# Kernel tuning notes

Hardware: AMD Instinct MI355X
Metric: run time of the kernel (lower is better)

Reference implementation:

```python
import jax, jax.numpy as jnp
import numpy as np


def setup_inputs() -> dict:
    key = jax.random.key(0)
    kq, kk, kv = jax.random.split(key, 3)
    n, m, d, v = 4096, 4096, 1024, 1024
    Q = jax.random.normal(kq, (n, d), dtype=jnp.float32)
    K = jax.random.normal(kk, (m, d), dtype=jnp.float32)
    V = jax.random.normal(kv, (m, v), dtype=jnp.float32)
    return {"Q": Q, "K": K, "V": V}


def reference(Q, K, V):
    d = K.shape[-1]
    scale = d ** (-0.5)
    logits = jnp.matmul(Q, K.T)                      # [n, m]
    # Faithful to source: softmax over dim=1 (keys), THEN scaled by d**-0.5
    scores = jax.nn.softmax(logits, axis=1) * scale  # [n, m]
    return jnp.matmul(scores, V)                     # [n, v]
```

## Files before the change

kernel.cpp:

```cpp
#include <hip/hip_runtime.h>
#include <hip/hip_bf16.h>

typedef _Float16 f16x8 __attribute__((ext_vector_type(8)));
typedef _Float16 f16x4 __attribute__((ext_vector_type(4)));
typedef float f32x4 __attribute__((ext_vector_type(4)));

__device__ __forceinline__ void async_ld16(_Float16* lds, const _Float16* g) {
    __builtin_amdgcn_global_load_lds(
        (const __attribute__((address_space(1))) void*)g,
        (__attribute__((address_space(3))) void*)lds, 16, 0, 0);
}

__global__ __launch_bounds__(256) void gemm_bt(
    const _Float16* __restrict__ A,
    const _Float16* __restrict__ B,
    float* __restrict__ C,
    int M, int N, int K, int Ks)
{
    __shared__ _Float16 At[2][128 * 32];
    __shared__ _Float16 Bt[2][128 * 32];

    const int tid  = threadIdx.x;
    const int wave = tid >> 6;
    const int lane = tid & 63;

    int gx = gridDim.x, gy = gridDim.y;
    int bx = blockIdx.x, by = blockIdx.y;
    if (((gx & 7) == 0) && ((gy & 7) == 0)) {
        const int bid    = bx + gx * by;
        const int ntx    = gx >> 3;
        const int sid    = bid >> 6;
        const int within = bid & 63;
        const int sx = sid % ntx;
        const int sy = sid / ntx;
        bx = (sx << 3) + (within & 7);
        by = (sy << 3) + (within >> 3);
    }
    const int row0 = by * 128;
    const int col0 = bx * 128;

    const int wr = (wave >> 1) * 64;
    const int wc = (wave & 1) * 64;
    const int quad = lane >> 4;
    const int l16  = lane & 15;

    f32x4 acc[4][4] = {};

    const int srow  = lane >> 2;
    const int skoff = (lane & 3) * 8;
    const size_t K64 = (size_t)64 * K;

    const _Float16* Ab = A + (size_t)row0 * K + (size_t)blockIdx.z * Ks;
    const _Float16* Bb = B + (size_t)col0 * K + (size_t)blockIdx.z * Ks;
    float* Cb = C + (size_t)blockIdx.z * M * N;

    const _Float16* pa = Ab + (size_t)(wave * 16 + srow) * K + skoff;
    const _Float16* pb = Bb + (size_t)(wave * 16 + srow) * K + skoff;

    async_ld16(At[0] + wave * 512,       pa);
    async_ld16(At[0] + (wave + 4) * 512, pa + K64);
    async_ld16(Bt[0] + wave * 512,       pb);
    async_ld16(Bt[0] + (wave + 4) * 512, pb + K64);
    __syncthreads();

    int cur = 0;
    for (int k0 = 0; k0 < Ks; k0 += 32) {
        const int nxt = cur ^ 1;
        if (k0 + 32 < Ks) {
            const _Float16* qa = pa + k0 + 32;
            const _Float16* qb = pb + k0 + 32;
            async_ld16(At[nxt] + wave * 512,       qa);
            async_ld16(At[nxt] + (wave + 4) * 512, qa + K64);
            async_ld16(Bt[nxt] + wave * 512,       qb);
            async_ld16(Bt[nxt] + (wave + 4) * 512, qb + K64);
        }

        f16x8 af[4], bf[4];
        #pragma unroll
        for (int r = 0; r < 4; ++r)
            af[r] = *(const f16x8*)&At[cur][(wr + r * 16 + l16) * 32 + quad * 8];
        #pragma unroll
        for (int c = 0; c < 4; ++c)
            bf[c] = *(const f16x8*)&Bt[cur][(wc + c * 16 + l16) * 32 + quad * 8];

        #pragma unroll
        for (int r = 0; r < 4; ++r)
            #pragma unroll
            for (int c = 0; c < 4; ++c)
                acc[r][c] = __builtin_amdgcn_mfma_f32_16x16x32_f16(af[r], bf[c], acc[r][c], 0, 0, 0);

        __syncthreads();
        cur = nxt;
    }

    #pragma unroll
    for (int r = 0; r < 4; ++r) {
        const int growb = row0 + wr + r * 16 + quad * 4;
        #pragma unroll
        for (int c = 0; c < 4; ++c) {
            const int gcol = col0 + wc + c * 16 + l16;
            #pragma unroll
            for (int i = 0; i < 4; ++i)
                Cb[(size_t)(growb + i) * N + gcol] = acc[r][c][i];
        }
    }
}

__global__ __launch_bounds__(256) void softmax_rows(
    const float* __restrict__ S, _Float16* __restrict__ P, float scale)
{
    __shared__ float red[4];
    const int row = blockIdx.x;
    const int tid = threadIdx.x;
    const int wave = tid >> 6;
    const float4* Sr = (const float4*)(S + (size_t)row * 4096);

    float4 x[4];
    #pragma unroll
    for (int i = 0; i < 4; ++i) x[i] = Sr[tid + i * 256];

    float mx = -3.402823466e+38f;
    #pragma unroll
    for (int i = 0; i < 4; ++i)
        mx = fmaxf(mx, fmaxf(fmaxf(x[i].x, x[i].y), fmaxf(x[i].z, x[i].w)));
    #pragma unroll
    for (int off = 32; off > 0; off >>= 1) mx = fmaxf(mx, __shfl_down(mx, off));
    if ((tid & 63) == 0) red[wave] = mx;
    __syncthreads();
    mx = fmaxf(fmaxf(red[0], red[1]), fmaxf(red[2], red[3]));
    __syncthreads();

    float sum = 0.0f;
    #pragma unroll
    for (int i = 0; i < 4; ++i) {
        x[i].x = __expf(x[i].x - mx);
        x[i].y = __expf(x[i].y - mx);
        x[i].z = __expf(x[i].z - mx);
        x[i].w = __expf(x[i].w - mx);
        sum += x[i].x + x[i].y + x[i].z + x[i].w;
    }
    #pragma unroll
    for (int off = 32; off > 0; off >>= 1) sum += __shfl_down(sum, off);
    if ((tid & 63) == 0) red[wave] = sum;
    __syncthreads();
    sum = red[0] + red[1] + red[2] + red[3];

    const float inv = scale / sum;
    f16x4* Pr = (f16x4*)(P + (size_t)row * 4096);
    #pragma unroll
    for (int i = 0; i < 4; ++i) {
        f16x4 h;
        h.x = (_Float16)(x[i].x * inv);
        h.y = (_Float16)(x[i].y * inv);
        h.z = (_Float16)(x[i].z * inv);
        h.w = (_Float16)(x[i].w * inv);
        Pr[tid + i * 256] = h;
    }
}

__global__ __launch_bounds__(256) void cvt2_f32_f16(
    const float4* __restrict__ a, f16x4* __restrict__ da, int n4a,
    const float4* __restrict__ b, f16x4* __restrict__ db, int n4b)
{
    int i = blockIdx.x * 256 + threadIdx.x;
    const int stride = gridDim.x * 256;
    const int tot = n4a + n4b;
    for (; i < tot; i += stride) {
        const float4* s = (i < n4a) ? (a + i) : (b + (i - n4a));
        f16x4* d = (i < n4a) ? (da + i) : (db + (i - n4a));
        float4 v = *s;
        f16x4 h;
        h.x = (_Float16)v.x; h.y = (_Float16)v.y;
        h.z = (_Float16)v.z; h.w = (_Float16)v.w;
        *d = h;
    }
}

__global__ __launch_bounds__(256) void transpose_cvt(
    const float* __restrict__ V, _Float16* __restrict__ Vt, int rows, int cols)
{
    __shared__ float tile[32][33];
    const int c0 = blockIdx.x * 32;
    const int r0 = blockIdx.y * 32;
    const int tx = threadIdx.x & 31;
    const int ty = threadIdx.x >> 5;
    #pragma unroll
    for (int i = 0; i < 4; ++i)
        tile[ty * 4 + i][tx] = V[(size_t)(r0 + ty * 4 + i) * cols + c0 + tx];
    __syncthreads();
    #pragma unroll
    for (int i = 0; i < 4; ++i)
        Vt[(size_t)(c0 + ty * 4 + i) * rows + r0 + tx] = (_Float16)tile[tx][ty * 4 + i];
}

__global__ __launch_bounds__(256) void reduce2(
    const float4* __restrict__ a, const float4* __restrict__ b,
    float4* __restrict__ o, int n4)
{
    int i = blockIdx.x * 256 + threadIdx.x;
    const int stride = gridDim.x * 256;
    for (; i < n4; i += stride) {
        float4 u = a[i], v = b[i];
        float4 w;
        w.x = u.x + v.x; w.y = u.y + v.y; w.z = u.z + v.z; w.w = u.w + v.w;
        o[i] = w;
    }
}

extern "C" void kernel_launch(void* const* d_in, const int* in_sizes, int n_in,
                              void* d_out, int out_size, void* d_ws, size_t ws_size,
                              hipStream_t stream) {
    const float* Q = (const float*)d_in[0];
    const float* K = (const float*)d_in[1];
    const float* V = (const float*)d_in[2];
    float* out = (float*)d_out;

    const int n = 4096, m = 4096, d = 1024, vdim = 1024;
    const float scale = 0.03125f;

    char* w = (char*)d_ws;
    _Float16* Qh = (_Float16*)w;
    _Float16* Kh = (_Float16*)(w + (8u << 20));
    _Float16* Vt = (_Float16*)(w + (16u << 20));
    char* rest = w + (24u << 20);
    size_t avail = ws_size > (24u << 20) ? ws_size - (24u << 20) : 0;

    int nc = 128;
    if      ((size_t)4096 * m * 6 <= avail) nc = 4096;
    else if ((size_t)2048 * m * 6 <= avail) nc = 2048;
    else if ((size_t)1024 * m * 6 <= avail) nc = 1024;
    else if ((size_t)512  * m * 6 <= avail) nc = 512;
    else if ((size_t)256  * m * 6 <= avail) nc = 256;

    float*    S = (float*)rest;
    _Float16* P = (_Float16*)(rest + (size_t)nc * m * 4);
    float* part = S;

    cvt2_f32_f16<<<dim3(2048), dim3(256), 0, stream>>>(
        (const float4*)Q, (f16x4*)Qh, n * d / 4,
        (const float4*)K, (f16x4*)Kh, m * d / 4);
    transpose_cvt<<<dim3(vdim / 32, m / 32), dim3(256), 0, stream>>>(V, Vt, m, vdim);

    for (int r0 = 0; r0 < n; r0 += nc) {
        gemm_bt<<<dim3(m / 128, nc / 128, 1), dim3(256), 0, stream>>>(
            Qh + (size_t)r0 * d, Kh, S, nc, m, d, d);
        softmax_rows<<<dim3(nc), dim3(256), 0, stream>>>(S, P, scale);
        gemm_bt<<<dim3(vdim / 128, nc / 128, 2), dim3(256), 0, stream>>>(
            P, Vt, part, nc, vdim, m, m / 2);
        reduce2<<<dim3(1024), dim3(256), 0, stream>>>(
            (const float4*)part, (const float4*)(part + (size_t)nc * vdim),
            (float4*)(out + (size_t)r0 * vdim), nc * vdim / 4);
    }
}
```

Baseline: 213.4 us.

## Write softmax fp16 in place and split-K partials into free workspace slack

Softmax now writes its fp16 probabilities in place over the fp32 logits buffer, reading it back with a doubled row stride, so no separate P buffer is needed. Split-K partial results go through per-slice output descriptors: slice 0 writes straight into the final output, and the other slices land in the unused upper half of each S row or in spare workspace. The reduction adds the remaining partials onto the output in place. This cuts workspace needs and allows larger row chunks and more K-splits (up to 4) when workspace is limited. The cost is strided, less cache-friendly fp16 reads and more complicated pointer handling.

```diff
diff --git a/kernel.cpp b/kernel.cpp
--- a/kernel.cpp
+++ b/kernel.cpp
@@ -11,11 +11,15 @@
         (__attribute__((address_space(3))) void*)lds, 16, 0, 0);
 }
 
+struct CDesc {
+    float *p0, *p1, *p2, *p3;
+    int l0, l1, l2, l3;
+};
+
 __global__ __launch_bounds__(256) void gemm_bt(
     const _Float16* __restrict__ A,
     const _Float16* __restrict__ B,
-    float* __restrict__ C,
-    int M, int N, int K, int Ks)
+    int M, int N, int Ks, int lda, int ldb, CDesc cd)
 {
     __shared__ _Float16 At[2][128 * 32];
     __shared__ _Float16 Bt[2][128 * 32];
@@ -48,19 +52,20 @@
 
     const int srow  = lane >> 2;
     const int skoff = (lane & 3) * 8;
-    const size_t K64 = (size_t)64 * K;
-
-    const _Float16* Ab = A + (size_t)row0 * K + (size_t)blockIdx.z * Ks;
-    const _Float16* Bb = B + (size_t)col0 * K + (size_t)blockIdx.z * Ks;
-    float* Cb = C + (size_t)blockIdx.z * M * N;
-
-    const _Float16* pa = Ab + (size_t)(wave * 16 + srow) * K + skoff;
-    const _Float16* pb = Bb + (size_t)(wave * 16 + srow) * K + skoff;
+    const size_t K64a = (size_t)64 * lda;
+    const size_t K64b = (size_t)64 * ldb;
+
+    const int z = blockIdx.z;
+    const _Float16* Ab = A + (size_t)row0 * lda + (size_t)z * Ks;
+    const _Float16* Bb = B + (size_t)col0 * ldb + (size_t)z * Ks;
+
+    const _Float16* pa = Ab + (size_t)(wave * 16 + srow) * lda + skoff;
+    const _Float16* pb = Bb + (size_t)(wave * 16 + srow) * ldb + skoff;
 
     async_ld16(At[0] + wave * 512,       pa);
-    async_ld16(At[0] + (wave + 4) * 512, pa + K64);
+    async_ld16(At[0] + (wave + 4) * 512, pa + K64a);
     async_ld16(Bt[0] + wave * 512,       pb);
-    async_ld16(Bt[0] + (wave + 4) * 512, pb + K64);
+    async_ld16(Bt[0] + (wave + 4) * 512, pb + K64b);
     __syncthreads();
 
     int cur = 0;
@@ -70,9 +75,9 @@
             const _Float16* qa = pa + k0 + 32;
             const _Float16* qb = pb + k0 + 32;
             async_ld16(At[nxt] + wave * 512,       qa);
-            async_ld16(At[nxt] + (wave + 4) * 512, qa + K64);
+            async_ld16(At[nxt] + (wave + 4) * 512, qa + K64a);
             async_ld16(Bt[nxt] + wave * 512,       qb);
-            async_ld16(Bt[nxt] + (wave + 4) * 512, qb + K64);
+            async_ld16(Bt[nxt] + (wave + 4) * 512, qb + K64b);
         }
 
         f16x8 af[4], bf[4];
@@ -93,6 +98,12 @@
         cur = nxt;
     }
 
+    float* Cb; int ldc;
+    if      (z == 0) { Cb = cd.p0; ldc = cd.l0; }
+    else if (z == 1) { Cb = cd.p1; ldc = cd.l1; }
+    else if (z == 2) { Cb = cd.p2; ldc = cd.l2; }
+    else             { Cb = cd.p3; ldc = cd.l3; }
+
     #pragma unroll
     for (int r = 0; r < 4; ++r) {
         const int growb = row0 + wr + r * 16 + quad * 4;
@@ -101,13 +112,13 @@
             const int gcol = col0 + wc + c * 16 + l16;
             #pragma unroll
             for (int i = 0; i < 4; ++i)
-                Cb[(size_t)(growb + i) * N + gcol] = acc[r][c][i];
+                Cb[(size_t)(growb + i) * ldc + gcol] = acc[r][c][i];
         }
     }
 }
 
 __global__ __launch_bounds__(256) void softmax_rows(
-    const float* __restrict__ S, _Float16* __restrict__ P, float scale)
+    float* __restrict__ S, float scale)
 {
     __shared__ float red[4];
     const int row = blockIdx.x;
@@ -146,7 +157,7 @@
     sum = red[0] + red[1] + red[2] + red[3];
 
     const float inv = scale / sum;
-    f16x4* Pr = (f16x4*)(P + (size_t)row * 4096);
+    f16x4* Pr = (f16x4*)((_Float16*)S + (size_t)row * 8192);
     #pragma unroll
     for (int i = 0; i < 4; ++i) {
         f16x4 h;
@@ -193,17 +204,30 @@
         Vt[(size_t)(c0 + ty * 4 + i) * rows + r0 + tx] = (_Float16)tile[tx][ty * 4 + i];
 }
 
-__global__ __launch_bounds__(256) void reduce2(
-    const float4* __restrict__ a, const float4* __restrict__ b,
-    float4* __restrict__ o, int n4)
+__global__ __launch_bounds__(256) void reduce_add(
+    float4* __restrict__ out,
+    const float* __restrict__ p1, int ld1,
+    const float* __restrict__ p2, int ld2,
+    const float* __restrict__ p3, int ld3,
+    int nparts, int rows)
 {
     int i = blockIdx.x * 256 + threadIdx.x;
     const int stride = gridDim.x * 256;
-    for (; i < n4; i += stride) {
-        float4 u = a[i], v = b[i];
-        float4 w;
-        w.x = u.x + v.x; w.y = u.y + v.y; w.z = u.z + v.z; w.w = u.w + v.w;
-        o[i] = w;
+    const int tot = rows * 256;
+    for (; i < tot; i += stride) {
+        const int r = i >> 8, c = i & 255;
+        float4 v = out[i];
+        float4 a = ((const float4*)(p1 + (size_t)r * ld1))[c];
+        v.x += a.x; v.y += a.y; v.z += a.z; v.w += a.w;
+        if (nparts > 1) {
+            float4 b = ((const float4*)(p2 + (size_t)r * ld2))[c];
+            v.x += b.x; v.y += b.y; v.z += b.z; v.w += b.w;
+        }
+        if (nparts > 2) {
+            float4 d = ((const float4*)(p3 + (size_t)r * ld3))[c];
+            v.x += d.x; v.y += d.y; v.z += d.z; v.w += d.w;
+        }
+        out[i] = v;
     }
 }
 
@@ -225,16 +249,16 @@
     char* rest = w + (24u << 20);
     size_t avail = ws_size > (24u << 20) ? ws_size - (24u << 20) : 0;
 
-    int nc = 128;
-    if      ((size_t)4096 * m * 6 <= avail) nc = 4096;
-    else if ((size_t)2048 * m * 6 <= avail) nc = 2048;
-    else if ((size_t)1024 * m * 6 <= avail) nc = 1024;
-    else if ((size_t)512  * m * 6 <= avail) nc = 512;
-    else if ((size_t)256  * m * 6 <= avail) nc = 256;
-
-    float*    S = (float*)rest;
-    _Float16* P = (_Float16*)(rest + (size_t)nc * m * 4);
-    float* part = S;
+    int nc, sk;
+    if      (avail >= (size_t)4096 * 16384)                        { nc = 4096; sk = 2; }
+    else if (avail >= (size_t)2048 * 16384 + (size_t)2048 * 4096)  { nc = 2048; sk = 4; }
+    else if (avail >= (size_t)1024 * 16384 + (size_t)1024 * 4096)  { nc = 1024; sk = 4; }
+    else                                                           { nc = 512;  sk = 4; }
+
+    float* S = (float*)rest;
+    float* pd1 = S + 2048;
+    float* pd2 = S + 3072;
+    float* pde = S + (size_t)nc * 4096;
 
     cvt2_f32_f16<<<dim3(2048), dim3(256), 0, stream>>>(
         (const float4*)Q, (f16x4*)Qh, n * d / 4,
@@ -242,13 +266,23 @@
     transpose_cvt<<<dim3(vdim / 32, m / 32), dim3(256), 0, stream>>>(V, Vt, m, vdim);
 
     for (int r0 = 0; r0 < n; r0 += nc) {
+        CDesc cs; cs.p0 = S; cs.l0 = m;
+        cs.p1 = cs.p2 = cs.p3 = S; cs.l1 = cs.l2 = cs.l3 = m;
         gemm_bt<<<dim3(m / 128, nc / 128, 1), dim3(256), 0, stream>>>(
-            Qh + (size_t)r0 * d, Kh, S, nc, m, d, d);
-        softmax_rows<<<dim3(nc), dim3(256), 0, stream>>>(S, P, scale);
-        gemm_bt<<<dim3(vdim / 128, nc / 128, 2), dim3(256), 0, stream>>>(
-            P, Vt, part, nc, vdim, m, m / 2);
-        reduce2<<<dim3(1024), dim3(256), 0, stream>>>(
-            (const float4*)part, (const float4*)(part + (size_t)nc * vdim),
-            (float4*)(out + (size_t)r0 * vdim), nc * vdim / 4);
-    }
-}
+            Qh + (size_t)r0 * d, Kh, nc, m, d, d, d, cs);
+
+        softmax_rows<<<dim3(nc), dim3(256), 0, stream>>>(S, scale);
+
+        float* o0 = out + (size_t)r0 * vdim;
+        CDesc co;
+        co.p0 = o0;  co.l0 = vdim;
+        co.p1 = pd1; co.l1 = 4096;
+        co.p2 = pd2; co.l2 = 4096;
+        co.p3 = pde; co.l3 = vdim;
+        gemm_bt<<<dim3(vdim / 128, nc / 128, sk), dim3(256), 0, stream>>>(
+            (const _Float16*)S, Vt, nc, vdim, m / sk, 2 * m, m, co);
+
+        reduce_add<<<dim3(1024), dim3(256), 0, stream>>>(
+            (float4*)o0, pd1, 4096, pd2, 4096, pde, vdim, sk - 1, nc);
+    }
+}
```

New measurement: 216.4 us. Within noise of the previous version (+1.4%).
